# Performance work log

Hardware: AMD Instinct MI355X
Metric: run time of the kernel (lower is better)

Reference implementation:

```python
import jax, jax.numpy as jnp
import numpy as np

HEADS = 4
DIM_HEAD = 128
SCALE = DIM_HEAD ** (-0.5)


def setup_inputs() -> dict:
    key = jax.random.key(0)
    k1, k2 = jax.random.split(key)
    fmap = jax.random.normal(k1, (1, 256, 64, 64), dtype=jnp.float32)
    # 1x1 conv weight, no bias: [out_channels=2*heads*dim_head, in_channels=dim]
    W_qk = jax.random.normal(k2, (1024, 256), dtype=jnp.float32) * (256 ** -0.5)
    return {"fmap": fmap, "W_qk": W_qk}


def reference(fmap, W_qk):
    b, c, h, w = fmap.shape
    # 1x1 conv == channel-wise matmul
    qk = jnp.einsum('bcxy,oc->boxy', fmap, W_qk)  # [b, 2*heads*dim_head, h, w]
    q, k = jnp.split(qk, 2, axis=1)
    def to_bhxyd(t):
        # 'b (h d) x y -> b h x y d'
        return t.reshape(b, HEADS, DIM_HEAD, h, w).transpose(0, 1, 3, 4, 2)
    q = to_bhxyd(q) * SCALE
    k = to_bhxyd(k)
    sim = jnp.einsum('bhxyd,bhuvd->bhxyuv', q, k)
    sim = sim.reshape(b, HEADS, h * w, h * w)
    return jax.nn.softmax(sim, axis=-1)
```

## Files before the change

### kernel.cpp

```cpp
#include <hip/hip_runtime.h>
#include <math.h>

#define HEADS 4
#define DHEAD 128
#define NPOS  4096
#define CIN   256
#define SCALEF 0.08838834764831845f

typedef _Float16 half8  __attribute__((ext_vector_type(8)));
typedef _Float16 half4  __attribute__((ext_vector_type(4)));
typedef _Float16 half2v __attribute__((ext_vector_type(2)));
typedef float    f32x4  __attribute__((ext_vector_type(4)));

#define FRAG_HEAD_HALVES (256 * 4 * 512)

__global__ __launch_bounds__(256) void cvt_kernel(const float* __restrict__ fmap,
                                                  const float* __restrict__ W,
                                                  _Float16* __restrict__ W16,
                                                  _Float16* __restrict__ fmapT) {
  if (blockIdx.x < 16) {
    int base = blockIdx.x * 16384 + threadIdx.x;
#pragma unroll
    for (int t = 0; t < 64; ++t) {
      int idx = base + t * 256;
      float v = W[idx];
      W16[idx] = (_Float16)(idx < 512 * CIN ? v * SCALEF : v);
    }
  } else {
    int tile = blockIdx.x - 16;
    int p0 = (tile >> 2) * 64, c0 = (tile & 3) * 64;
    __shared__ float t_lds[64][65];
    int tid = threadIdx.x;
#pragma unroll
    for (int t = 0; t < 16; ++t) {
      int lin = tid + t * 256;
      int r = lin >> 6, col = lin & 63;
      t_lds[r][col] = fmap[(size_t)(c0 + r) * NPOS + p0 + col];
    }
    __syncthreads();
#pragma unroll
    for (int t = 0; t < 16; ++t) {
      int lin = tid + t * 256;
      int pr = lin >> 6, cc = lin & 63;
      fmapT[(size_t)(p0 + pr) * CIN + c0 + cc] = (_Float16)t_lds[cc][pr];
    }
  }
}

__global__ __launch_bounds__(256) void proj_mfma(const _Float16* __restrict__ W16,
                                                 const _Float16* __restrict__ fmapT,
                                                 _Float16* __restrict__ qf,
                                                 _Float16* __restrict__ kf) {
  const int p0 = blockIdx.x * 64;
  const int o0 = blockIdx.y * 64 + (threadIdx.x >> 6) * 16;
  const int l = threadIdx.x & 63;
  const int lr = l & 15, lg = l >> 4;

  const f32x4 z = {0.f, 0.f, 0.f, 0.f};
  f32x4 acc[4] = {z, z, z, z};
#pragma unroll
  for (int kb = 0; kb < 8; ++kb) {
    half8 a = *(const half8*)(W16 + (size_t)(o0 + lr) * CIN + kb * 32 + lg * 8);
#pragma unroll
    for (int j = 0; j < 4; ++j) {
      half8 b = *(const half8*)(fmapT + (size_t)(p0 + j * 16 + lr) * CIN + kb * 32 + lg * 8);
      acc[j] = __builtin_amdgcn_mfma_f32_16x16x32_f16(a, b, acc[j], 0, 0, 0);
    }
  }
  const int ob = o0 + lg * 4;
  const bool isq = ob < 512;
  const int oo = isq ? ob : ob - 512;
  const int h = oo >> 7, db = oo & 127;
  const int kb2 = db >> 5;
  const int flane = ((db >> 3) & 3) * 16 + lr;
  const int e0 = db & 7;
  _Float16* dst = (isq ? qf : kf) + (size_t)h * FRAG_HEAD_HALVES;
#pragma unroll
  for (int j = 0; j < 4; ++j) {
    int pt = (p0 >> 4) + j;
    half4 v = {(_Float16)acc[j][0], (_Float16)acc[j][1],
               (_Float16)acc[j][2], (_Float16)acc[j][3]};
    *(half4*)(dst + ((size_t)pt * 4 + kb2) * 512 + flane * 8 + e0) = v;
  }
}

#define QROWS 16
#define WCOLS 512
#define NTIL  32

__global__ __launch_bounds__(512) void attn_mfma(const _Float16* __restrict__ qf,
                                                 const _Float16* __restrict__ kf,
                                                 float* __restrict__ out) {
  const int h = blockIdx.y;
  const int i0 = blockIdx.x * QROWS;
  const int wv = threadIdx.x >> 6;
  const int l = threadIdx.x & 63;
  const int lr = l & 15, lg = l >> 4;

  const _Float16* Qf = qf + (size_t)h * FRAG_HEAD_HALVES;
  const _Float16* Kf = kf + (size_t)h * FRAG_HEAD_HALVES;

  half8 afr[4];
#pragma unroll
  for (int kb = 0; kb < 4; ++kb)
    afr[kb] = *(const half8*)(Qf + ((size_t)(i0 >> 4) * 4 + kb) * 512 + l * 8);

  const int jt0 = wv * NTIL;
  half2v Pst[2 * NTIL];
  float rs[4] = {0.f, 0.f, 0.f, 0.f};
  const f32x4 z = {0.f, 0.f, 0.f, 0.f};

#pragma unroll
  for (int t = 0; t < NTIL; ++t) {
    const _Float16* kp = Kf + ((size_t)(jt0 + t) * 4) * 512 + l * 8;
    f32x4 acc = z;
#pragma unroll
    for (int kb = 0; kb < 4; ++kb) {
      half8 b = *(const half8*)(kp + kb * 512);
      acc = __builtin_amdgcn_mfma_f32_16x16x32_f16(afr[kb], b, acc, 0, 0, 0);
    }
    float e0 = __expf(acc[0]);
    float e1 = __expf(acc[1]);
    float e2 = __expf(acc[2]);
    float e3 = __expf(acc[3]);
    rs[0] += e0; rs[1] += e1; rs[2] += e2; rs[3] += e3;
    half2v lo = {(_Float16)e0, (_Float16)e1};
    half2v hi = {(_Float16)e2, (_Float16)e3};
    Pst[2 * t] = lo;
    Pst[2 * t + 1] = hi;
  }

#pragma unroll
  for (int off = 1; off < 16; off <<= 1) {
#pragma unroll
    for (int r = 0; r < 4; ++r) rs[r] += __shfl_xor(rs[r], off);
  }
  __shared__ float red[8][16];
  if (lr == 0) {
#pragma unroll
    for (int r = 0; r < 4; ++r) red[wv][lg * 4 + r] = rs[r];
  }
  __syncthreads();
  float inv[4];
#pragma unroll
  for (int r = 0; r < 4; ++r) {
    float s = 0.f;
#pragma unroll
    for (int w = 0; w < 8; ++w) s += red[w][lg * 4 + r];
    inv[r] = 1.0f / s;
  }

  float* ob = out + ((size_t)h * NPOS + i0) * NPOS + jt0 * 16;
#pragma unroll
  for (int t = 0; t < NTIL; ++t) {
    half2v lo = Pst[2 * t];
    half2v hi = Pst[2 * t + 1];
    float e[4] = {(float)lo[0], (float)lo[1], (float)hi[0], (float)hi[1]};
#pragma unroll
    for (int r = 0; r < 4; ++r) {
      ob[(size_t)(lg * 4 + r) * NPOS + t * 16 + lr] = e[r] * inv[r];
    }
  }
}

extern "C" void kernel_launch(void* const* d_in, const int* in_sizes, int n_in,
                              void* d_out, int out_size, void* d_ws, size_t ws_size,
                              hipStream_t stream) {
  const float* fmap = (const float*)d_in[0];
  const float* W    = (const float*)d_in[1];
  float* out = (float*)d_out;

  char* ws = (char*)d_ws;
  _Float16* qf    = (_Float16*)(ws);
  _Float16* kf    = (_Float16*)(ws + (4u << 20));
  _Float16* W16   = (_Float16*)(ws + (8u << 20));
  _Float16* fmapT = (_Float16*)(ws + (8u << 20) + (512u << 10));

  cvt_kernel<<<272, 256, 0, stream>>>(fmap, W, W16, fmapT);
  proj_mfma<<<dim3(NPOS / 64, 1024 / 64), 256, 0, stream>>>(W16, fmapT, qf, kf);
  attn_mfma<<<dim3(NPOS / QROWS, HEADS), 512, 0, stream>>>(qf, kf, out);
}
```

Measured before the change: 111.5 us.

## Process two query row tiles per attention block to reuse K fragments

The attention kernel now handles 32 query rows per block instead of 16, loading each K fragment once and feeding it to two MFMA chains, one per 16-row tile. This halves K global loads per output and interleaves independent MFMAs for better latency hiding. The cost is roughly double the per-thread register use for stored probabilities and accumulators (128 half2 values), which can lower occupancy or cause spills. The grid is also halved.

```diff
diff --git a/kernel.cpp b/kernel.cpp
--- a/kernel.cpp
+++ b/kernel.cpp
@@ -84,8 +84,7 @@
   }
 }
 
-#define QROWS 16
-#define WCOLS 512
+#define QROWS 32
 #define NTIL  32
 
 __global__ __launch_bounds__(512) void attn_mfma(const _Float16* __restrict__ qf,
@@ -100,65 +99,92 @@
   const _Float16* Qf = qf + (size_t)h * FRAG_HEAD_HALVES;
   const _Float16* Kf = kf + (size_t)h * FRAG_HEAD_HALVES;
 
-  half8 afr[4];
-#pragma unroll
-  for (int kb = 0; kb < 4; ++kb)
-    afr[kb] = *(const half8*)(Qf + ((size_t)(i0 >> 4) * 4 + kb) * 512 + l * 8);
+  const int rtA = i0 >> 4;
+  half8 afrA[4], afrB[4];
+#pragma unroll
+  for (int kb = 0; kb < 4; ++kb) {
+    afrA[kb] = *(const half8*)(Qf + ((size_t)rtA * 4 + kb) * 512 + l * 8);
+    afrB[kb] = *(const half8*)(Qf + ((size_t)(rtA + 1) * 4 + kb) * 512 + l * 8);
+  }
 
   const int jt0 = wv * NTIL;
-  half2v Pst[2 * NTIL];
-  float rs[4] = {0.f, 0.f, 0.f, 0.f};
+  half2v PA[2 * NTIL];
+  half2v PB[2 * NTIL];
+  float rsA[4] = {0.f, 0.f, 0.f, 0.f};
+  float rsB[4] = {0.f, 0.f, 0.f, 0.f};
   const f32x4 z = {0.f, 0.f, 0.f, 0.f};
 
 #pragma unroll
   for (int t = 0; t < NTIL; ++t) {
     const _Float16* kp = Kf + ((size_t)(jt0 + t) * 4) * 512 + l * 8;
-    f32x4 acc = z;
-#pragma unroll
-    for (int kb = 0; kb < 4; ++kb) {
-      half8 b = *(const half8*)(kp + kb * 512);
-      acc = __builtin_amdgcn_mfma_f32_16x16x32_f16(afr[kb], b, acc, 0, 0, 0);
-    }
-    float e0 = __expf(acc[0]);
-    float e1 = __expf(acc[1]);
-    float e2 = __expf(acc[2]);
-    float e3 = __expf(acc[3]);
-    rs[0] += e0; rs[1] += e1; rs[2] += e2; rs[3] += e3;
-    half2v lo = {(_Float16)e0, (_Float16)e1};
-    half2v hi = {(_Float16)e2, (_Float16)e3};
-    Pst[2 * t] = lo;
-    Pst[2 * t + 1] = hi;
+    half8 b0 = *(const half8*)(kp);
+    half8 b1 = *(const half8*)(kp + 512);
+    half8 b2 = *(const half8*)(kp + 1024);
+    half8 b3 = *(const half8*)(kp + 1536);
+    f32x4 aA = z, aB = z;
+    aA = __builtin_amdgcn_mfma_f32_16x16x32_f16(afrA[0], b0, aA, 0, 0, 0);
+    aB = __builtin_amdgcn_mfma_f32_16x16x32_f16(afrB[0], b0, aB, 0, 0, 0);
+    aA = __builtin_amdgcn_mfma_f32_16x16x32_f16(afrA[1], b1, aA, 0, 0, 0);
+    aB = __builtin_amdgcn_mfma_f32_16x16x32_f16(afrB[1], b1, aB, 0, 0, 0);
+    aA = __builtin_amdgcn_mfma_f32_16x16x32_f16(afrA[2], b2, aA, 0, 0, 0);
+    aB = __builtin_amdgcn_mfma_f32_16x16x32_f16(afrB[2], b2, aB, 0, 0, 0);
+    aA = __builtin_amdgcn_mfma_f32_16x16x32_f16(afrA[3], b3, aA, 0, 0, 0);
+    aB = __builtin_amdgcn_mfma_f32_16x16x32_f16(afrB[3], b3, aB, 0, 0, 0);
+
+    float eA0 = __expf(aA[0]), eA1 = __expf(aA[1]);
+    float eA2 = __expf(aA[2]), eA3 = __expf(aA[3]);
+    float eB0 = __expf(aB[0]), eB1 = __expf(aB[1]);
+    float eB2 = __expf(aB[2]), eB3 = __expf(aB[3]);
+    rsA[0] += eA0; rsA[1] += eA1; rsA[2] += eA2; rsA[3] += eA3;
+    rsB[0] += eB0; rsB[1] += eB1; rsB[2] += eB2; rsB[3] += eB3;
+    PA[2 * t]     = half2v{(_Float16)eA0, (_Float16)eA1};
+    PA[2 * t + 1] = half2v{(_Float16)eA2, (_Float16)eA3};
+    PB[2 * t]     = half2v{(_Float16)eB0, (_Float16)eB1};
+    PB[2 * t + 1] = half2v{(_Float16)eB2, (_Float16)eB3};
   }
 
 #pragma unroll
   for (int off = 1; off < 16; off <<= 1) {
 #pragma unroll
-    for (int r = 0; r < 4; ++r) rs[r] += __shfl_xor(rs[r], off);
-  }
-  __shared__ float red[8][16];
+    for (int r = 0; r < 4; ++r) {
+      rsA[r] += __shfl_xor(rsA[r], off);
+      rsB[r] += __shfl_xor(rsB[r], off);
+    }
+  }
+  __shared__ float red[8][32];
   if (lr == 0) {
 #pragma unroll
-    for (int r = 0; r < 4; ++r) red[wv][lg * 4 + r] = rs[r];
+    for (int r = 0; r < 4; ++r) {
+      red[wv][lg * 4 + r] = rsA[r];
+      red[wv][16 + lg * 4 + r] = rsB[r];
+    }
   }
   __syncthreads();
-  float inv[4];
+  float invA[4], invB[4];
 #pragma unroll
   for (int r = 0; r < 4; ++r) {
-    float s = 0.f;
-#pragma unroll
-    for (int w = 0; w < 8; ++w) s += red[w][lg * 4 + r];
-    inv[r] = 1.0f / s;
-  }
-
-  float* ob = out + ((size_t)h * NPOS + i0) * NPOS + jt0 * 16;
+    float sA = 0.f, sB = 0.f;
+#pragma unroll
+    for (int w = 0; w < 8; ++w) {
+      sA += red[w][lg * 4 + r];
+      sB += red[w][16 + lg * 4 + r];
+    }
+    invA[r] = 1.0f / sA;
+    invB[r] = 1.0f / sB;
+  }
+
+  float* obA = out + ((size_t)h * NPOS + i0) * NPOS + jt0 * 16;
+  float* obB = obA + (size_t)16 * NPOS;
 #pragma unroll
   for (int t = 0; t < NTIL; ++t) {
-    half2v lo = Pst[2 * t];
-    half2v hi = Pst[2 * t + 1];
-    float e[4] = {(float)lo[0], (float)lo[1], (float)hi[0], (float)hi[1]};
+    float eA[4] = {(float)PA[2 * t][0], (float)PA[2 * t][1],
+                   (float)PA[2 * t + 1][0], (float)PA[2 * t + 1][1]};
+    float eB[4] = {(float)PB[2 * t][0], (float)PB[2 * t][1],
+                   (float)PB[2 * t + 1][0], (float)PB[2 * t + 1][1]};
 #pragma unroll
     for (int r = 0; r < 4; ++r) {
-      ob[(size_t)(lg * 4 + r) * NPOS + t * 16 + lr] = e[r] * inv[r];
+      obA[(size_t)(lg * 4 + r) * NPOS + t * 16 + lr] = eA[r] * invA[r];
+      obB[(size_t)(lg * 4 + r) * NPOS + t * 16 + lr] = eB[r] * invB[r];
     }
   }
 }
```

Result: slower. 134.5 us (+20.5%).
